# Kernel tuning notes

Measured on AMD Instinct MI355X. Metric: run time of the kernel, lower is better.

The kernel has to match this reference:

```python
import jax, jax.numpy as jnp
import numpy as np

QMAX = 127.0  # 8-bit symmetric: levels in [-128, 127]


def _ste_round(v):
    # round with straight-through estimator (matches torch fake-quant training)
    return v + jax.lax.stop_gradient(jnp.round(v) - v)


def _act_fake_quant(x, clip_factor):
    # per-tensor symmetric fake quant with learnable clip (lac):
    # clip range = sigmoid(clip_factor) * max|x|
    scale = jax.nn.sigmoid(clip_factor) * jnp.max(jnp.abs(x)) / QMAX
    return jnp.clip(_ste_round(x / scale), -QMAX - 1.0, QMAX) * scale


def _weight_fake_quant(w):
    # per-output-channel symmetric fake quant; w: [out, in]
    scale = jnp.max(jnp.abs(w), axis=1, keepdims=True) / QMAX
    return jnp.clip(_ste_round(w / scale), -QMAX - 1.0, QMAX) * scale


def setup_inputs() -> dict:
    key = jax.random.key(0)
    k1, k2, k3, k4 = jax.random.split(key, 4)
    B, S, H, I = 8, 8192, 1024, 2816
    return {
        "x": jax.random.normal(k1, (B, S, H), dtype=jnp.float32),
        "clip_x": jnp.full((1,), 4.0, dtype=jnp.float32),     # sigmoid(4) ~ 0.982
        "clip_down": jnp.full((1,), 4.0, dtype=jnp.float32),
        "w_gate": jax.random.normal(k2, (I, H), dtype=jnp.float32) * 0.02,
        "w_up": jax.random.normal(k3, (I, H), dtype=jnp.float32) * 0.02,
        "w_down": jax.random.normal(k4, (H, I), dtype=jnp.float32) * 0.02,
    }


def reference(x, clip_x, clip_down, w_gate, w_up, w_down):
    # _trans_forward: quantize act -> gate/up quant-matmul -> SwiGLU -> quantize -> down quant-matmul
    xq = _act_fake_quant(x, clip_x[0])                       # [B,S,H]
    gate = jnp.einsum("bsh,ih->bsi", xq, _weight_fake_quant(w_gate))
    up = jnp.einsum("bsh,ih->bsi", xq, _weight_fake_quant(w_up))
    h = _act_fake_quant(jax.nn.silu(gate) * up, clip_down[0])  # [B,S,I]
    return jnp.einsum("bsi,hi->bsh", h, _weight_fake_quant(w_down))
```

## Files before the change

kernel.cpp:

```cpp
#include <hip/hip_runtime.h>
#include <stdint.h>

typedef __attribute__((ext_vector_type(4))) int i32x4;

typedef const __attribute__((address_space(1))) void gvoid_t;
typedef __attribute__((address_space(3))) void lvoid_t;

#define GLD16(g, l) __builtin_amdgcn_global_load_lds((gvoid_t*)(g), (lvoid_t*)(l), 16, 0, 0)
#define FENCE() asm volatile("" ::: "memory")
#define BARRIER() do { FENCE(); __builtin_amdgcn_s_barrier(); FENCE(); } while (0)

__device__ inline int q1mul(float x, float r) {
    return (int)fminf(fmaxf(rintf(x * r), -128.f), 127.f);
}
__device__ inline int q1div(float x, float s) {
    return (int)fminf(fmaxf(rintf(x / s), -128.f), 127.f);
}
__device__ inline int pack4(float4 v, float r) {
    return (q1mul(v.x, r) & 255) | ((q1mul(v.y, r) & 255) << 8) |
           ((q1mul(v.z, r) & 255) << 16) | ((q1mul(v.w, r) & 255) << 24);
}

__global__ void k_absmax(const float* __restrict__ x, size_t n4, unsigned int* __restrict__ out) {
    size_t S = (size_t)gridDim.x * blockDim.x;
    size_t i = (size_t)blockIdx.x * blockDim.x + threadIdx.x;
    const float4* x4 = (const float4*)x;
    float m = 0.f;
    for (; i + 3 * S < n4; i += 4 * S) {
        float4 v0 = x4[i], v1 = x4[i + S], v2 = x4[i + 2 * S], v3 = x4[i + 3 * S];
        m = fmaxf(m, fmaxf(fmaxf(fabsf(v0.x), fabsf(v0.y)), fmaxf(fabsf(v0.z), fabsf(v0.w))));
        m = fmaxf(m, fmaxf(fmaxf(fabsf(v1.x), fabsf(v1.y)), fmaxf(fabsf(v1.z), fabsf(v1.w))));
        m = fmaxf(m, fmaxf(fmaxf(fabsf(v2.x), fabsf(v2.y)), fmaxf(fabsf(v2.z), fabsf(v2.w))));
        m = fmaxf(m, fmaxf(fmaxf(fabsf(v3.x), fabsf(v3.y)), fmaxf(fabsf(v3.z), fabsf(v3.w))));
    }
    for (; i < n4; i += S) {
        float4 v = x4[i];
        m = fmaxf(m, fmaxf(fmaxf(fabsf(v.x), fabsf(v.y)), fmaxf(fabsf(v.z), fabsf(v.w))));
    }
    #pragma unroll
    for (int off = 32; off > 0; off >>= 1) m = fmaxf(m, __shfl_xor(m, off, 64));
    if ((threadIdx.x & 63) == 0) atomicMax(out, __float_as_uint(m));
}

__global__ void k_scale(const float* __restrict__ clip, const unsigned int* __restrict__ maxbits,
                        float* __restrict__ s_out) {
    float m = __uint_as_float(*maxbits);
    float sig = 1.f / (1.f + expf(-clip[0]));
    float s = sig * m / 127.f;
    s_out[0] = s;
    s_out[1] = 1.f / s;
}

__global__ void k_quant_f32_i8(const float* __restrict__ in, int4* __restrict__ out,
                               const float* __restrict__ sptr, size_t n16) {
    float r = sptr[1];
    size_t S = (size_t)gridDim.x * blockDim.x;
    size_t i = (size_t)blockIdx.x * blockDim.x + threadIdx.x;
    const float4* in4 = (const float4*)in;
    for (; i < n16; i += S) {
        float4 v0 = in4[4 * i], v1 = in4[4 * i + 1], v2 = in4[4 * i + 2], v3 = in4[4 * i + 3];
        int4 o;
        o.x = pack4(v0, r); o.y = pack4(v1, r); o.z = pack4(v2, r); o.w = pack4(v3, r);
        out[i] = o;
    }
}

__global__ void k_quant_w_i8(const float* __restrict__ W, int8_t* __restrict__ Q,
                             float* __restrict__ srow, int cols) {
    int row = blockIdx.x;
    const float* w = W + (size_t)row * cols;
    float m = 0.f;
    for (int c = threadIdx.x; c < cols; c += 256) m = fmaxf(m, fabsf(w[c]));
    #pragma unroll
    for (int off = 32; off > 0; off >>= 1) m = fmaxf(m, __shfl_xor(m, off, 64));
    __shared__ float red[4];
    if ((threadIdx.x & 63) == 0) red[threadIdx.x >> 6] = m;
    __syncthreads();
    if (threadIdx.x == 0) {
        float mm = fmaxf(fmaxf(red[0], red[1]), fmaxf(red[2], red[3]));
        red[0] = mm / 127.f;
        srow[row] = mm / 127.f;
    }
    __syncthreads();
    float s = red[0];
    for (int c = threadIdx.x; c < cols; c += 256)
        Q[(size_t)row * cols + c] = (int8_t)q1div(w[c], s);
}

__global__ __launch_bounds__(512, 2) void k_gemm1_i8(
    const int8_t* __restrict__ Aq, const int8_t* __restrict__ Bg, const int8_t* __restrict__ Bu,
    const float* __restrict__ sg, const float* __restrict__ su, const float* __restrict__ sx,
    float* __restrict__ Hout, unsigned int* __restrict__ maxh)
{
    constexpr int K = 1024, N = 2816, NT = K / 64, TB = 32768;
    __shared__ int8_t lds[3 * TB];

    const int ntn = N / 128;
    const int chunk = gridDim.x >> 3;
    const int wg = ((int)blockIdx.x & 7) * chunk + ((int)blockIdx.x >> 3);
    const int mt = wg / ntn, nt = wg % ntn;
    const int m0 = mt * 256, n0 = nt * 128;
    const int tid = threadIdx.x;
    const int wid = tid >> 6, lane = tid & 63;
    const int wm = wid >> 2, wn = wid & 3;
    const int lr = lane & 15, lk = lane >> 4;

    const int srow = tid >> 2;
    const int scol = ((tid & 3) ^ ((srow >> 1) & 3)) << 4;
    const int8_t* gA0 = Aq + (size_t)(m0 + srow) * K + scol;
    const int8_t* gA1 = gA0 + (size_t)128 * K;
    const int8_t* gG  = Bg + (size_t)(n0 + srow) * K + scol;
    const int8_t* gU  = Bu + (size_t)(n0 + srow) * K + scol;
    const int ldst = wid << 10;

    const int swz = (lk ^ ((lr >> 1) & 3)) << 4;
    int offA[8], offG[2], offU[2];
    #pragma unroll
    for (int mi = 0; mi < 8; ++mi) offA[mi] = (wm * 128 + mi * 16 + lr) * 64 + swz;
    #pragma unroll
    for (int ni = 0; ni < 2; ++ni) {
        offG[ni] = 16384 + (wn * 32 + ni * 16 + lr) * 64 + swz;
        offU[ni] = 24576 + (wn * 32 + ni * 16 + lr) * 64 + swz;
    }

    i32x4 accg[8][2] = {};
    i32x4 accu[8][2] = {};

    {
        int8_t* L0 = &lds[0];
        GLD16(gA0, L0 + ldst);          GLD16(gA1, L0 + 8192 + ldst);
        GLD16(gG,  L0 + 16384 + ldst);  GLD16(gU,  L0 + 24576 + ldst);
        int8_t* L1 = &lds[TB];
        GLD16(gA0 + 64, L1 + ldst);          GLD16(gA1 + 64, L1 + 8192 + ldst);
        GLD16(gG  + 64, L1 + 16384 + ldst);  GLD16(gU  + 64, L1 + 24576 + ldst);
    }
    asm volatile("s_waitcnt vmcnt(4)" ::: "memory");
    BARRIER();

    for (int t = 0; t < NT; ++t) {
        const int8_t* L = &lds[(t % 3) * TB];
        int8_t* Ls = &lds[((t + 2) % 3) * TB];
        const size_t k2 = (size_t)(t + 2) * 64;
        const bool st = (t + 2 < NT);

        i32x4 a[4], bgf[2], buf_[2];
        #pragma unroll
        for (int mi = 0; mi < 4; ++mi) a[mi] = *(const i32x4*)(L + offA[mi]);
        #pragma unroll
        for (int ni = 0; ni < 2; ++ni) {
            bgf[ni]  = *(const i32x4*)(L + offG[ni]);
            buf_[ni] = *(const i32x4*)(L + offU[ni]);
        }
        if (st) { GLD16(gA0 + k2, Ls + ldst); GLD16(gA1 + k2, Ls + 8192 + ldst); }
        BARRIER();
        __builtin_amdgcn_s_setprio(1);
        #pragma unroll
        for (int mi = 0; mi < 4; ++mi) {
            #pragma unroll
            for (int ni = 0; ni < 2; ++ni) {
                accg[mi][ni] = __builtin_amdgcn_mfma_i32_16x16x64_i8(a[mi], bgf[ni], accg[mi][ni], 0, 0, 0);
                accu[mi][ni] = __builtin_amdgcn_mfma_i32_16x16x64_i8(a[mi], buf_[ni], accu[mi][ni], 0, 0, 0);
            }
        }
        __builtin_amdgcn_s_setprio(0);
        BARRIER();

        i32x4 a2[4];
        #pragma unroll
        for (int mi = 0; mi < 4; ++mi) a2[mi] = *(const i32x4*)(L + offA[4 + mi]);
        if (st) { GLD16(gG + k2, Ls + 16384 + ldst); GLD16(gU + k2, Ls + 24576 + ldst); }
        BARRIER();
        __builtin_amdgcn_s_setprio(1);
        #pragma unroll
        for (int mi = 0; mi < 4; ++mi) {
            #pragma unroll
            for (int ni = 0; ni < 2; ++ni) {
                accg[4 + mi][ni] = __builtin_amdgcn_mfma_i32_16x16x64_i8(a2[mi], bgf[ni], accg[4 + mi][ni], 0, 0, 0);
                accu[4 + mi][ni] = __builtin_amdgcn_mfma_i32_16x16x64_i8(a2[mi], buf_[ni], accu[4 + mi][ni], 0, 0, 0);
            }
        }
        __builtin_amdgcn_s_setprio(0);
        if (st) { asm volatile("s_waitcnt vmcnt(4)" ::: "memory"); }
        else    { asm volatile("s_waitcnt vmcnt(0)" ::: "memory"); }
        BARRIER();
    }

    const float s_x = sx[0];
    float lmax = 0.f;
    #pragma unroll
    for (int ni = 0; ni < 2; ++ni) {
        const int n = n0 + wn * 32 + ni * 16 + lr;
        const float fg = s_x * sg[n];
        const float fu = s_x * su[n];
        #pragma unroll
        for (int mi = 0; mi < 8; ++mi) {
            const int mb = m0 + wm * 128 + mi * 16 + lk * 4;
            #pragma unroll
            for (int r = 0; r < 4; ++r) {
                float g = (float)accg[mi][ni][r] * fg;
                float u = (float)accu[mi][ni][r] * fu;
                float h = g * u / (1.f + expf(-g));
                Hout[(size_t)(mb + r) * N + n] = h;
                lmax = fmaxf(lmax, fabsf(h));
            }
        }
    }
    #pragma unroll
    for (int off = 32; off > 0; off >>= 1) lmax = fmaxf(lmax, __shfl_xor(lmax, off, 64));
    if (lane == 0) atomicMax(maxh, __float_as_uint(lmax));
}

__global__ __launch_bounds__(512, 2) void k_gemm2_i8(
    const int8_t* __restrict__ Aq, const int8_t* __restrict__ Bw,
    const float* __restrict__ sw, const float* __restrict__ sh,
    float* __restrict__ Out)
{
    constexpr int K = 2816, N = 1024, NT = K / 64, TB = 32768;
    __shared__ int8_t lds[3 * TB];

    const int chunk = gridDim.x >> 3;
    const int wg = ((int)blockIdx.x & 7) * chunk + ((int)blockIdx.x >> 3);
    const int mt = wg >> 2, nt = wg & 3;
    const int m0 = mt * 256, n0 = nt * 256;
    const int tid = threadIdx.x;
    const int wid = tid >> 6, lane = tid & 63;
    const int wm = wid >> 2, wn = wid & 3;
    const int lr = lane & 15, lk = lane >> 4;

    const int srow = tid >> 2;
    const int scol = ((tid & 3) ^ ((srow >> 1) & 3)) << 4;
    const int8_t* gA0 = Aq + (size_t)(m0 + srow) * K + scol;
    const int8_t* gA1 = gA0 + (size_t)128 * K;
    const int8_t* gB0 = Bw + (size_t)(n0 + srow) * K + scol;
    const int8_t* gB1 = gB0 + (size_t)128 * K;
    const int ldst = wid << 10;

    const int swz = (lk ^ ((lr >> 1) & 3)) << 4;
    int offA[8], offB[4];
    #pragma unroll
    for (int mi = 0; mi < 8; ++mi) offA[mi] = (wm * 128 + mi * 16 + lr) * 64 + swz;
    #pragma unroll
    for (int ni = 0; ni < 4; ++ni) offB[ni] = 16384 + (wn * 64 + ni * 16 + lr) * 64 + swz;

    i32x4 acc[8][4] = {};

    {
        int8_t* L0 = &lds[0];
        GLD16(gA0, L0 + ldst);          GLD16(gA1, L0 + 8192 + ldst);
        GLD16(gB0, L0 + 16384 + ldst);  GLD16(gB1, L0 + 24576 + ldst);
        int8_t* L1 = &lds[TB];
        GLD16(gA0 + 64, L1 + ldst);          GLD16(gA1 + 64, L1 + 8192 + ldst);
        GLD16(gB0 + 64, L1 + 16384 + ldst);  GLD16(gB1 + 64, L1 + 24576 + ldst);
    }
    asm volatile("s_waitcnt vmcnt(4)" ::: "memory");
    BARRIER();

    for (int t = 0; t < NT; ++t) {
        const int8_t* L = &lds[(t % 3) * TB];
        int8_t* Ls = &lds[((t + 2) % 3) * TB];
        const size_t k2 = (size_t)(t + 2) * 64;
        const bool st = (t + 2 < NT);

        i32x4 a[4], b[4];
        #pragma unroll
        for (int mi = 0; mi < 4; ++mi) a[mi] = *(const i32x4*)(L + offA[mi]);
        #pragma unroll
        for (int ni = 0; ni < 4; ++ni) b[ni] = *(const i32x4*)(L + offB[ni]);
        if (st) { GLD16(gA0 + k2, Ls + ldst); GLD16(gA1 + k2, Ls + 8192 + ldst); }
        BARRIER();
        __builtin_amdgcn_s_setprio(1);
        #pragma unroll
        for (int mi = 0; mi < 4; ++mi) {
            #pragma unroll
            for (int ni = 0; ni < 4; ++ni)
                acc[mi][ni] = __builtin_amdgcn_mfma_i32_16x16x64_i8(a[mi], b[ni], acc[mi][ni], 0, 0, 0);
        }
        __builtin_amdgcn_s_setprio(0);
        BARRIER();

        i32x4 a2[4];
        #pragma unroll
        for (int mi = 0; mi < 4; ++mi) a2[mi] = *(const i32x4*)(L + offA[4 + mi]);
        if (st) { GLD16(gB0 + k2, Ls + 16384 + ldst); GLD16(gB1 + k2, Ls + 24576 + ldst); }
        BARRIER();
        __builtin_amdgcn_s_setprio(1);
        #pragma unroll
        for (int mi = 0; mi < 4; ++mi) {
            #pragma unroll
            for (int ni = 0; ni < 4; ++ni)
                acc[4 + mi][ni] = __builtin_amdgcn_mfma_i32_16x16x64_i8(a2[mi], b[ni], acc[4 + mi][ni], 0, 0, 0);
        }
        __builtin_amdgcn_s_setprio(0);
        if (st) { asm volatile("s_waitcnt vmcnt(4)" ::: "memory"); }
        else    { asm volatile("s_waitcnt vmcnt(0)" ::: "memory"); }
        BARRIER();
    }

    const float s_h = sh[0];
    #pragma unroll
    for (int ni = 0; ni < 4; ++ni) {
        const int n = n0 + wn * 64 + ni * 16 + lr;
        const float f = s_h * sw[n];
        #pragma unroll
        for (int mi = 0; mi < 8; ++mi) {
            const int mb = m0 + wm * 128 + mi * 16 + lk * 4;
            #pragma unroll
            for (int r = 0; r < 4; ++r)
                Out[(size_t)(mb + r) * N + n] = (float)acc[mi][ni][r] * f;
        }
    }
}

extern "C" void kernel_launch(void* const* d_in, const int* in_sizes, int n_in,
                              void* d_out, int out_size, void* d_ws, size_t ws_size,
                              hipStream_t stream) {
    const float* x       = (const float*)d_in[0];
    const float* clip_x  = (const float*)d_in[1];
    const float* clip_dn = (const float*)d_in[2];
    const float* w_gate  = (const float*)d_in[3];
    const float* w_up    = (const float*)d_in[4];
    const float* w_down  = (const float*)d_in[5];
    float* out = (float*)d_out;

    const int Hd = 1024, Id = 2816;
    const int M = in_sizes[0] / Hd;
    const size_t nx = (size_t)M * Hd;
    const size_t nh = (size_t)M * Id;

    char* ws = (char*)d_ws;
    size_t off = 0;
    auto alloc = [&](size_t bytes) -> char* {
        char* p = ws + off;
        off = (off + bytes + 255) & ~(size_t)255;
        return p;
    };
    unsigned int* max_slots = (unsigned int*)alloc(8);
    float* sxp = (float*)alloc(8);
    float* shp = (float*)alloc(8);
    int8_t* qx  = (int8_t*)alloc(nx);
    int8_t* qwg = (int8_t*)alloc((size_t)Id * Hd);
    int8_t* qwu = (int8_t*)alloc((size_t)Id * Hd);
    int8_t* qwd = (int8_t*)alloc((size_t)Hd * Id);
    float* swg = (float*)alloc((size_t)Id * 4);
    float* swu = (float*)alloc((size_t)Id * 4);
    float* swd = (float*)alloc((size_t)Hd * 4);
    int8_t* qh = (int8_t*)alloc(nh);
    float* hbuf = (float*)alloc(nh * 4);

    hipMemsetAsync(max_slots, 0, 8, stream);

    k_absmax<<<4096, 256, 0, stream>>>(x, nx / 4, &max_slots[0]);
    k_scale<<<1, 1, 0, stream>>>(clip_x, &max_slots[0], sxp);
    k_quant_f32_i8<<<2048, 256, 0, stream>>>(x, (int4*)qx, sxp, nx / 16);
    k_quant_w_i8<<<Id, 256, 0, stream>>>(w_gate, qwg, swg, Hd);
    k_quant_w_i8<<<Id, 256, 0, stream>>>(w_up, qwu, swu, Hd);
    k_quant_w_i8<<<Hd, 256, 0, stream>>>(w_down, qwd, swd, Id);

    k_gemm1_i8<<<(M / 256) * (Id / 128), 512, 0, stream>>>(qx, qwg, qwu, swg, swu, sxp,
                                                           hbuf, &max_slots[1]);
    k_scale<<<1, 1, 0, stream>>>(clip_dn, &max_slots[1], shp);
    k_quant_f32_i8<<<4096, 256, 0, stream>>>(hbuf, (int4*)qh, shp, nh / 16);

    k_gemm2_i8<<<(M / 256) * (Hd / 256), 512, 0, stream>>>(qh, qwd, swd, shp, out);
}
```

Before: 1.382 ms.

## Switch int8 GEMMs to double-buffered 128-wide K stages

Both int8 GEMM kernels move from a triple-buffered pipeline of 64-wide K tiles to a double-buffered pipeline of 128-wide K stages, each split into two 64-wide halves with staggered global-to-LDS loads. This halves the number of outer loop iterations and changes how prefetch distance and vmcnt waits line up with the MFMA phases. LDS use grows from 96KB to 128KB per block, which may limit occupancy at launch_bounds(512,2), and the prefetch distance in K elements is now tied to stage size.

```diff
diff --git a/kernel.cpp b/kernel.cpp
--- a/kernel.cpp
+++ b/kernel.cpp
@@ -9,6 +9,8 @@
 #define GLD16(g, l) __builtin_amdgcn_global_load_lds((gvoid_t*)(g), (lvoid_t*)(l), 16, 0, 0)
 #define FENCE() asm volatile("" ::: "memory")
 #define BARRIER() do { FENCE(); __builtin_amdgcn_s_barrier(); FENCE(); } while (0)
+#define VMCNT4() asm volatile("s_waitcnt vmcnt(4)" ::: "memory")
+#define VMCNT0() asm volatile("s_waitcnt vmcnt(0)" ::: "memory")
 
 __device__ inline int q1mul(float x, float r) {
     return (int)fminf(fmaxf(rintf(x * r), -128.f), 127.f);
@@ -92,8 +94,8 @@
     const float* __restrict__ sg, const float* __restrict__ su, const float* __restrict__ sx,
     float* __restrict__ Hout, unsigned int* __restrict__ maxh)
 {
-    constexpr int K = 1024, N = 2816, NT = K / 64, TB = 32768;
-    __shared__ int8_t lds[3 * TB];
+    constexpr int K = 1024, N = 2816, NT = K / 128, BUF = 65536;
+    __shared__ int8_t lds[2 * BUF];
 
     const int ntn = N / 128;
     const int chunk = gridDim.x >> 3;
@@ -114,74 +116,101 @@
     const int ldst = wid << 10;
 
     const int swz = (lk ^ ((lr >> 1) & 3)) << 4;
-    int offA[8], offG[2], offU[2];
-    #pragma unroll
-    for (int mi = 0; mi < 8; ++mi) offA[mi] = (wm * 128 + mi * 16 + lr) * 64 + swz;
-    #pragma unroll
-    for (int ni = 0; ni < 2; ++ni) {
-        offG[ni] = 16384 + (wn * 32 + ni * 16 + lr) * 64 + swz;
-        offU[ni] = 24576 + (wn * 32 + ni * 16 + lr) * 64 + swz;
-    }
 
     i32x4 accg[8][2] = {};
     i32x4 accu[8][2] = {};
 
     {
-        int8_t* L0 = &lds[0];
-        GLD16(gA0, L0 + ldst);          GLD16(gA1, L0 + 8192 + ldst);
-        GLD16(gG,  L0 + 16384 + ldst);  GLD16(gU,  L0 + 24576 + ldst);
-        int8_t* L1 = &lds[TB];
-        GLD16(gA0 + 64, L1 + ldst);          GLD16(gA1 + 64, L1 + 8192 + ldst);
-        GLD16(gG  + 64, L1 + 16384 + ldst);  GLD16(gU  + 64, L1 + 24576 + ldst);
-    }
-    asm volatile("s_waitcnt vmcnt(4)" ::: "memory");
+        int8_t* Lw = &lds[0];
+        GLD16(gA0,      Lw + ldst);         GLD16(gA1,      Lw + 8192  + ldst);
+        GLD16(gG,       Lw + 32768 + ldst); GLD16(gU,       Lw + 40960 + ldst);
+        GLD16(gA0 + 64, Lw + 16384 + ldst); GLD16(gA1 + 64, Lw + 24576 + ldst);
+        GLD16(gG  + 64, Lw + 49152 + ldst); GLD16(gU  + 64, Lw + 57344 + ldst);
+    }
+    VMCNT4();
     BARRIER();
 
     for (int t = 0; t < NT; ++t) {
-        const int8_t* L = &lds[(t % 3) * TB];
-        int8_t* Ls = &lds[((t + 2) % 3) * TB];
-        const size_t k2 = (size_t)(t + 2) * 64;
-        const bool st = (t + 2 < NT);
-
-        i32x4 a[4], bgf[2], buf_[2];
-        #pragma unroll
-        for (int mi = 0; mi < 4; ++mi) a[mi] = *(const i32x4*)(L + offA[mi]);
+        const bool st = (t + 1 < NT);
+        const size_t kk = (size_t)(t + 1) * 128;
+        const int8_t* Lr = &lds[(t & 1) * BUF];
+        int8_t* Lw = &lds[((t + 1) & 1) * BUF];
+        i32x4 a[4], bg[2], bu[2];
+
+        #pragma unroll
+        for (int mi = 0; mi < 4; ++mi)
+            a[mi] = *(const i32x4*)(Lr + (wm * 128 + mi * 16 + lr) * 64 + swz);
         #pragma unroll
         for (int ni = 0; ni < 2; ++ni) {
-            bgf[ni]  = *(const i32x4*)(L + offG[ni]);
-            buf_[ni] = *(const i32x4*)(L + offU[ni]);
+            bg[ni] = *(const i32x4*)(Lr + 32768 + (wn * 32 + ni * 16 + lr) * 64 + swz);
+            bu[ni] = *(const i32x4*)(Lr + 40960 + (wn * 32 + ni * 16 + lr) * 64 + swz);
         }
-        if (st) { GLD16(gA0 + k2, Ls + ldst); GLD16(gA1 + k2, Ls + 8192 + ldst); }
-        BARRIER();
-        __builtin_amdgcn_s_setprio(1);
-        #pragma unroll
-        for (int mi = 0; mi < 4; ++mi) {
+        if (st) { GLD16(gA0 + kk, Lw + ldst); GLD16(gA1 + kk, Lw + 8192 + ldst); }
+        BARRIER();
+        __builtin_amdgcn_s_setprio(1);
+        #pragma unroll
+        for (int mi = 0; mi < 4; ++mi)
             #pragma unroll
             for (int ni = 0; ni < 2; ++ni) {
-                accg[mi][ni] = __builtin_amdgcn_mfma_i32_16x16x64_i8(a[mi], bgf[ni], accg[mi][ni], 0, 0, 0);
-                accu[mi][ni] = __builtin_amdgcn_mfma_i32_16x16x64_i8(a[mi], buf_[ni], accu[mi][ni], 0, 0, 0);
+                accg[mi][ni] = __builtin_amdgcn_mfma_i32_16x16x64_i8(a[mi], bg[ni], accg[mi][ni], 0, 0, 0);
+                accu[mi][ni] = __builtin_amdgcn_mfma_i32_16x16x64_i8(a[mi], bu[ni], accu[mi][ni], 0, 0, 0);
             }
+        __builtin_amdgcn_s_setprio(0);
+        BARRIER();
+
+        #pragma unroll
+        for (int mi = 0; mi < 4; ++mi)
+            a[mi] = *(const i32x4*)(Lr + (wm * 128 + 64 + mi * 16 + lr) * 64 + swz);
+        if (st) { GLD16(gG + kk, Lw + 32768 + ldst); GLD16(gU + kk, Lw + 40960 + ldst); }
+        BARRIER();
+        __builtin_amdgcn_s_setprio(1);
+        #pragma unroll
+        for (int mi = 0; mi < 4; ++mi)
+            #pragma unroll
+            for (int ni = 0; ni < 2; ++ni) {
+                accg[4 + mi][ni] = __builtin_amdgcn_mfma_i32_16x16x64_i8(a[mi], bg[ni], accg[4 + mi][ni], 0, 0, 0);
+                accu[4 + mi][ni] = __builtin_amdgcn_mfma_i32_16x16x64_i8(a[mi], bu[ni], accu[4 + mi][ni], 0, 0, 0);
+            }
+        __builtin_amdgcn_s_setprio(0);
+        if (st) { VMCNT4(); } else { VMCNT0(); }
+        BARRIER();
+
+        #pragma unroll
+        for (int mi = 0; mi < 4; ++mi)
+            a[mi] = *(const i32x4*)(Lr + 16384 + (wm * 128 + mi * 16 + lr) * 64 + swz);
+        #pragma unroll
+        for (int ni = 0; ni < 2; ++ni) {
+            bg[ni] = *(const i32x4*)(Lr + 49152 + (wn * 32 + ni * 16 + lr) * 64 + swz);
+            bu[ni] = *(const i32x4*)(Lr + 57344 + (wn * 32 + ni * 16 + lr) * 64 + swz);
         }
-        __builtin_amdgcn_s_setprio(0);
-        BARRIER();
-
-        i32x4 a2[4];
-        #pragma unroll
-        for (int mi = 0; mi < 4; ++mi) a2[mi] = *(const i32x4*)(L + offA[4 + mi]);
-        if (st) { GLD16(gG + k2, Ls + 16384 + ldst); GLD16(gU + k2, Ls + 24576 + ldst); }
-        BARRIER();
-        __builtin_amdgcn_s_setprio(1);
-        #pragma unroll
-        for (int mi = 0; mi < 4; ++mi) {
+        if (st) { GLD16(gA0 + kk + 64, Lw + 16384 + ldst); GLD16(gA1 + kk + 64, Lw + 24576 + ldst); }
+        BARRIER();
+        __builtin_amdgcn_s_setprio(1);
+        #pragma unroll
+        for (int mi = 0; mi < 4; ++mi)
             #pragma unroll
             for (int ni = 0; ni < 2; ++ni) {
-                accg[4 + mi][ni] = __builtin_amdgcn_mfma_i32_16x16x64_i8(a2[mi], bgf[ni], accg[4 + mi][ni], 0, 0, 0);
-                accu[4 + mi][ni] = __builtin_amdgcn_mfma_i32_16x16x64_i8(a2[mi], buf_[ni], accu[4 + mi][ni], 0, 0, 0);
+                accg[mi][ni] = __builtin_amdgcn_mfma_i32_16x16x64_i8(a[mi], bg[ni], accg[mi][ni], 0, 0, 0);
+                accu[mi][ni] = __builtin_amdgcn_mfma_i32_16x16x64_i8(a[mi], bu[ni], accu[mi][ni], 0, 0, 0);
             }
-        }
-        __builtin_amdgcn_s_setprio(0);
-        if (st) { asm volatile("s_waitcnt vmcnt(4)" ::: "memory"); }
-        else    { asm volatile("s_waitcnt vmcnt(0)" ::: "memory"); }
+        __builtin_amdgcn_s_setprio(0);
+        BARRIER();
+
+        #pragma unroll
+        for (int mi = 0; mi < 4; ++mi)
+            a[mi] = *(const i32x4*)(Lr + 16384 + (wm * 128 + 64 + mi * 16 + lr) * 64 + swz);
+        if (st) { GLD16(gG + kk + 64, Lw + 49152 + ldst); GLD16(gU + kk + 64, Lw + 57344 + ldst); }
+        BARRIER();
+        __builtin_amdgcn_s_setprio(1);
+        #pragma unroll
+        for (int mi = 0; mi < 4; ++mi)
+            #pragma unroll
+            for (int ni = 0; ni < 2; ++ni) {
+                accg[4 + mi][ni] = __builtin_amdgcn_mfma_i32_16x16x64_i8(a[mi], bg[ni], accg[4 + mi][ni], 0, 0, 0);
+                accu[4 + mi][ni] = __builtin_amdgcn_mfma_i32_16x16x64_i8(a[mi], bu[ni], accu[4 + mi][ni], 0, 0, 0);
+            }
+        __builtin_amdgcn_s_setprio(0);
+        if (st) { VMCNT4(); }
         BARRIER();
     }
 
@@ -215,8 +244,8 @@
     const float* __restrict__ sw, const float* __restrict__ sh,
     float* __restrict__ Out)
 {
-    constexpr int K = 2816, N = 1024, NT = K / 64, TB = 32768;
-    __shared__ int8_t lds[3 * TB];
+    constexpr int K = 2816, N = 1024, NT = K / 128, BUF = 65536;
+    __shared__ int8_t lds[2 * BUF];
 
     const int chunk = gridDim.x >> 3;
     const int wg = ((int)blockIdx.x & 7) * chunk + ((int)blockIdx.x >> 3);
@@ -236,63 +265,88 @@
     const int ldst = wid << 10;
 
     const int swz = (lk ^ ((lr >> 1) & 3)) << 4;
-    int offA[8], offB[4];
-    #pragma unroll
-    for (int mi = 0; mi < 8; ++mi) offA[mi] = (wm * 128 + mi * 16 + lr) * 64 + swz;
-    #pragma unroll
-    for (int ni = 0; ni < 4; ++ni) offB[ni] = 16384 + (wn * 64 + ni * 16 + lr) * 64 + swz;
 
     i32x4 acc[8][4] = {};
 
     {
-        int8_t* L0 = &lds[0];
-        GLD16(gA0, L0 + ldst);          GLD16(gA1, L0 + 8192 + ldst);
-        GLD16(gB0, L0 + 16384 + ldst);  GLD16(gB1, L0 + 24576 + ldst);
-        int8_t* L1 = &lds[TB];
-        GLD16(gA0 + 64, L1 + ldst);          GLD16(gA1 + 64, L1 + 8192 + ldst);
-        GLD16(gB0 + 64, L1 + 16384 + ldst);  GLD16(gB1 + 64, L1 + 24576 + ldst);
-    }
-    asm volatile("s_waitcnt vmcnt(4)" ::: "memory");
+        int8_t* Lw = &lds[0];
+        GLD16(gA0,      Lw + ldst);         GLD16(gA1,      Lw + 8192  + ldst);
+        GLD16(gB0,      Lw + 32768 + ldst); GLD16(gB1,      Lw + 40960 + ldst);
+        GLD16(gA0 + 64, Lw + 16384 + ldst); GLD16(gA1 + 64, Lw + 24576 + ldst);
+        GLD16(gB0 + 64, Lw + 49152 + ldst); GLD16(gB1 + 64, Lw + 57344 + ldst);
+    }
+    VMCNT4();
     BARRIER();
 
     for (int t = 0; t < NT; ++t) {
-        const int8_t* L = &lds[(t % 3) * TB];
-        int8_t* Ls = &lds[((t + 2) % 3) * TB];
-        const size_t k2 = (size_t)(t + 2) * 64;
-        const bool st = (t + 2 < NT);
-
+        const bool st = (t + 1 < NT);
+        const size_t kk = (size_t)(t + 1) * 128;
+        const int8_t* Lr = &lds[(t & 1) * BUF];
+        int8_t* Lw = &lds[((t + 1) & 1) * BUF];
         i32x4 a[4], b[4];
-        #pragma unroll
-        for (int mi = 0; mi < 4; ++mi) a[mi] = *(const i32x4*)(L + offA[mi]);
-        #pragma unroll
-        for (int ni = 0; ni < 4; ++ni) b[ni] = *(const i32x4*)(L + offB[ni]);
-        if (st) { GLD16(gA0 + k2, Ls + ldst); GLD16(gA1 + k2, Ls + 8192 + ldst); }
-        BARRIER();
-        __builtin_amdgcn_s_setprio(1);
-        #pragma unroll
-        for (int mi = 0; mi < 4; ++mi) {
+
+        #pragma unroll
+        for (int mi = 0; mi < 4; ++mi)
+            a[mi] = *(const i32x4*)(Lr + (wm * 128 + mi * 16 + lr) * 64 + swz);
+        #pragma unroll
+        for (int ni = 0; ni < 4; ++ni)
+            b[ni] = *(const i32x4*)(Lr + 32768 + (wn * 64 + ni * 16 + lr) * 64 + swz);
+        if (st) { GLD16(gA0 + kk, Lw + ldst); GLD16(gA1 + kk, Lw + 8192 + ldst); }
+        BARRIER();
+        __builtin_amdgcn_s_setprio(1);
+        #pragma unroll
+        for (int mi = 0; mi < 4; ++mi)
             #pragma unroll
             for (int ni = 0; ni < 4; ++ni)
                 acc[mi][ni] = __builtin_amdgcn_mfma_i32_16x16x64_i8(a[mi], b[ni], acc[mi][ni], 0, 0, 0);
-        }
-        __builtin_amdgcn_s_setprio(0);
-        BARRIER();
-
-        i32x4 a2[4];
-        #pragma unroll
-        for (int mi = 0; mi < 4; ++mi) a2[mi] = *(const i32x4*)(L + offA[4 + mi]);
-        if (st) { GLD16(gB0 + k2, Ls + 16384 + ldst); GLD16(gB1 + k2, Ls + 24576 + ldst); }
-        BARRIER();
-        __builtin_amdgcn_s_setprio(1);
-        #pragma unroll
-        for (int mi = 0; mi < 4; ++mi) {
+        __builtin_amdgcn_s_setprio(0);
+        BARRIER();
+
+        #pragma unroll
+        for (int mi = 0; mi < 4; ++mi)
+            a[mi] = *(const i32x4*)(Lr + (wm * 128 + 64 + mi * 16 + lr) * 64 + swz);
+        if (st) { GLD16(gB0 + kk, Lw + 32768 + ldst); GLD16(gB1 + kk, Lw + 40960 + ldst); }
+        BARRIER();
+        __builtin_amdgcn_s_setprio(1);
+        #pragma unroll
+        for (int mi = 0; mi < 4; ++mi)
             #pragma unroll
             for (int ni = 0; ni < 4; ++ni)
-                acc[4 + mi][ni] = __builtin_amdgcn_mfma_i32_16x16x64_i8(a2[mi], b[ni], acc[4 + mi][ni], 0, 0, 0);
-        }
-        __builtin_amdgcn_s_setprio(0);
-        if (st) { asm volatile("s_waitcnt vmcnt(4)" ::: "memory"); }
-        else    { asm volatile("s_waitcnt vmcnt(0)" ::: "memory"); }
+                acc[4 + mi][ni] = __builtin_amdgcn_mfma_i32_16x16x64_i8(a[mi], b[ni], acc[4 + mi][ni], 0, 0, 0);
+        __builtin_amdgcn_s_setprio(0);
+        if (st) { VMCNT4(); } else { VMCNT0(); }
+        BARRIER();
+
+        #pragma unroll
+        for (int mi = 0; mi < 4; ++mi)
+            a[mi] = *(const i32x4*)(Lr + 16384 + (wm * 128 + mi * 16 + lr) * 64 + swz);
+        #pragma unroll
+        for (int ni = 0; ni < 4; ++ni)
+            b[ni] = *(const i32x4*)(Lr + 49152 + (wn * 64 + ni * 16 + lr) * 64 + swz);
+        if (st) { GLD16(gA0 + kk + 64, Lw + 16384 + ldst); GLD16(gA1 + kk + 64, Lw + 24576 + ldst); }
+        BARRIER();
+        __builtin_amdgcn_s_setprio(1);
+        #pragma unroll
+        for (int mi = 0; mi < 4; ++mi)
+            #pragma unroll
+            for (int ni = 0; ni < 4; ++ni)
+                acc[mi][ni] = __builtin_amdgcn_mfma_i32_16x16x64_i8(a[mi], b[ni], acc[mi][ni], 0, 0, 0);
+        __builtin_amdgcn_s_setprio(0);
+        BARRIER();
+
+        #pragma unroll
+        for (int mi = 0; mi < 4; ++mi)
+            a[mi] = *(const i32x4*)(Lr + 16384 + (wm * 128 + 64 + mi * 16 + lr) * 64 + swz);
+        if (st) { GLD16(gB0 + kk + 64, Lw + 49152 + ldst); GLD16(gB1 + kk + 64, Lw + 57344 + ldst); }
+        BARRIER();
+        __builtin_amdgcn_s_setprio(1);
+        #pragma unroll
+        for (int mi = 0; mi < 4; ++mi)
+            #pragma unroll
+            for (int ni = 0; ni < 4; ++ni)
+                acc[4 + mi][ni] = __builtin_amdgcn_mfma_i32_16x16x64_i8(a[mi], b[ni], acc[4 + mi][ni], 0, 0, 0);
+        __builtin_amdgcn_s_setprio(0);
+        if (st) { VMCNT4(); }
         BARRIER();
     }
 
```

Result: no change. 1.372 ms (-0.7%).
